# Optimization experiments

Measured on AMD Instinct MI355X. Metric: run time of the kernel, lower is better.

The kernel has to match this reference:

```python
import jax, jax.numpy as jnp
import numpy as np

HIDDEN = 2048
INTER = 4096
NUM_EXPERTS = 8
TOP_K = 4
BATCH, SEQ = 2, 2048
TOKENS = BATCH * SEQ


def setup_inputs() -> dict:
    key = jax.random.key(0)
    k_x, k_rw, k_tw, k_te, k_gu, k_dn = jax.random.split(key, 6)
    x = jax.random.normal(k_x, (BATCH, SEQ, HIDDEN), dtype=jnp.float32)
    # full router weights (passed through but unused by this patched forward)
    weights = jax.random.uniform(k_rw, (TOKENS, NUM_EXPERTS), dtype=jnp.float32)
    tw = jax.random.uniform(k_tw, (TOKENS, TOP_K), dtype=jnp.float32)
    top_weights = tw / jnp.sum(tw, axis=-1, keepdims=True)  # softmax-like, renormalize=False downstream
    top_experts = jax.random.randint(k_te, (TOKENS, TOP_K), 0, NUM_EXPERTS, dtype=jnp.int64)
    scale_gu = 1.0 / np.sqrt(HIDDEN)
    scale_dn = 1.0 / np.sqrt(INTER)
    gate_up_weights = jax.random.normal(k_gu, (NUM_EXPERTS, 2 * INTER, HIDDEN), dtype=jnp.float32) * scale_gu
    down_weights = jax.random.normal(k_dn, (NUM_EXPERTS, HIDDEN, INTER), dtype=jnp.float32) * scale_dn
    return {
        'x': x,
        'weights': weights,
        'top_weights': top_weights,
        'top_experts': top_experts,
        'gate_up_weights': gate_up_weights,
        'down_weights': down_weights,
    }


def _fused_moe(xf, gate_up_weights, down_weights, top_weights, top_experts):
    """xf: [T, D]. Dense per-expert loop (scan over experts), masked combine.

    Matches fused_moe(renormalize=False): out[t] = sum_k top_weights[t,k] * expert_{top_experts[t,k]}(x[t])
    expert(x) = (silu(x @ Wg^T) * (x @ Wu^T)) @ Wd^T with [Wg; Wu] = gate_up.
    """
    E = gate_up_weights.shape[0]

    def step(out, inp):
        w_gu, w_d, e = inp
        # per-token combine coefficient for this expert (0 if not routed)
        coef = jnp.sum(jnp.where(top_experts == e, top_weights, 0.0), axis=-1)  # [T]
        h = xf @ w_gu.T                       # [T, 2*INTER]
        gate, up = jnp.split(h, 2, axis=-1)
        act = jax.nn.silu(gate) * up          # [T, INTER]
        o = act @ w_d.T                       # [T, D]
        return out + coef[:, None] * o, None

    out, _ = jax.lax.scan(step, jnp.zeros_like(xf),
                          (gate_up_weights, down_weights, jnp.arange(E, dtype=jnp.int64)))
    return out


def reference(x, weights, top_weights, top_experts, gate_up_weights, down_weights):
    B, S, D = x.shape
    xf = x.reshape(-1, D)  # flatten(0, 1)
    out = _fused_moe(xf, gate_up_weights, down_weights, top_weights, top_experts)
    return out.reshape(B, S, D)  # unflatten(0, (-1, q_len))
```

## Files before the change

kernel.cpp:

```cpp
#include <hip/hip_runtime.h>
#include <stdint.h>

#define T_TOKENS 4096
#define D_HID    2048
#define D_INT    4096
#define N_EXP    8
#define TOPK     4
#define NFLAT    (T_TOKENS*TOPK)
#define BMT      256
#define MAXPAD   (NFLAT + N_EXP*BMT)
#define MT2      (MAXPAD/BMT)

#define OFF_PTOK 0ull
#define OFF_PWT  73728ull
#define OFF_CNT  147456ull
#define OFF_TOFF 147712ull
#define OFF_SEG  155904ull
#define OFF_XB   262144ull
#define OFF_ACT  17039360ull
#define OFF_W    168034304ull

typedef float f32x4  __attribute__((ext_vector_type(4)));
typedef short bf16x8 __attribute__((ext_vector_type(8)));

__device__ __forceinline__ unsigned short f2bf(float f) {
    unsigned int u = __float_as_uint(f);
    u += 0x7fffu + ((u >> 16) & 1u);
    return (unsigned short)(u >> 16);
}

__device__ __forceinline__ void gload_lds16(const void* g, void* l) {
    __builtin_amdgcn_global_load_lds((const __attribute__((address_space(1))) void*)g,
                                     (__attribute__((address_space(3))) void*)l,
                                     16, 0, 0);
}

__device__ __forceinline__ int xcd_logical(int hw, int nwg) {
    int q = nwg >> 3, r = nwg & 7;
    int xc = hw & 7, sl = hw >> 3;
    return (xc < r ? xc * (q + 1) : r * (q + 1) + (xc - r) * q) + sl;
}

__global__ void k_prep(const float* __restrict__ x, unsigned short* __restrict__ xb,
                       float* __restrict__ out) {
    const int N4 = T_TOKENS * D_HID / 4;
    for (int i = blockIdx.x * 256 + threadIdx.x; i < N4; i += 2048 * 256) {
        float4 v = ((const float4*)x)[i];
        ushort4 h;
        h.x = f2bf(v.x); h.y = f2bf(v.y); h.z = f2bf(v.z); h.w = f2bf(v.w);
        ((ushort4*)xb)[i] = h;
        ((float4*)out)[i] = make_float4(0.f, 0.f, 0.f, 0.f);
    }
}

__global__ void k_cast(const float* __restrict__ src, unsigned short* __restrict__ dst, int n4) {
    for (int i = blockIdx.x * 256 + threadIdx.x; i < n4; i += 2048 * 256) {
        float4 v = ((const float4*)src)[i];
        ushort4 h;
        h.x = f2bf(v.x); h.y = f2bf(v.y); h.z = f2bf(v.z); h.w = f2bf(v.w);
        ((ushort4*)dst)[i] = h;
    }
}

__global__ void k_count(const int* __restrict__ te, int* __restrict__ counts,
                        int* __restrict__ toff) {
    int e = blockIdx.x, t = threadIdx.x;
    int cnt = 0;
    int base = t * 64;
    for (int i = 0; i < 64; i++) cnt += (te[base + i] == e);
    __shared__ int s[256];
    s[t] = cnt; __syncthreads();
    int incl = cnt;
    for (int off = 1; off < 256; off <<= 1) {
        int tmp = (t >= off) ? s[t - off] : 0;
        __syncthreads();
        incl += tmp; s[t] = incl;
        __syncthreads();
    }
    toff[e * 256 + t] = incl - cnt;
    if (t == 255) counts[e] = incl;
}

__global__ void k_fill(const int* __restrict__ te, const float* __restrict__ tw,
                       const int* __restrict__ counts, const int* __restrict__ toff,
                       int* __restrict__ ptok, float* __restrict__ pwt, int* __restrict__ seg) {
    int e = blockIdx.x, t = threadIdx.x;
    int segs[9]; int a = 0;
    #pragma unroll
    for (int j = 0; j < 8; j++) { segs[j] = a; a += (counts[j] + BMT - 1) & ~(BMT - 1); }
    segs[8] = a;
    if (e == 0 && t == 0) { for (int j = 0; j < 9; j++) seg[j] = segs[j]; }
    int base = segs[e] + toff[e * 256 + t];
    int rank = 0;
    for (int i = t * 64; i < (t + 1) * 64; i++) {
        if (te[i] == e) { ptok[base + rank] = i >> 2; pwt[base + rank] = tw[i]; rank++; }
    }
    int cnt = counts[e], pc = (cnt + BMT - 1) & ~(BMT - 1);
    for (int i = cnt + t; i < pc; i += 256) { ptok[segs[e] + i] = -1; pwt[segs[e] + i] = 0.f; }
}


#define MFMA4(MI, AF) \
    _Pragma("unroll") for (int n_ = 0; n_ < 4; ++n_) \
        acc[MI][n_] = __builtin_amdgcn_mfma_f32_16x16x32_bf16(AF, bf[n_], acc[MI][n_], 0, 0, 0);

#define GBODY(VMS) \
  asm volatile("s_waitcnt vmcnt(" VMS ")" ::: "memory"); \
  __builtin_amdgcn_s_barrier(); \
  __builtin_amdgcn_sched_barrier(0); \
  { \
    const char* pT = ldsc + (cb << 15); \
    bf16x8 bf[4], af[4], ag[4]; \
    _Pragma("unroll") for (int n_ = 0; n_ < 4; ++n_) \
        bf[n_] = *(const bf16x8*)(pT + b_off + n_ * 1024); \
    _Pragma("unroll") for (int m_ = 0; m_ < 4; ++m_) \
        af[m_] = *(const bf16x8*)(pT + a_off + m_ * 1024); \
    __builtin_amdgcn_s_barrier(); \
    asm volatile("s_waitcnt lgkmcnt(0)" ::: "memory"); \
    __builtin_amdgcn_sched_barrier(0); \
    __builtin_amdgcn_s_setprio(1); \
    MFMA4(0, af[0]) MFMA4(1, af[1]) MFMA4(2, af[2]) MFMA4(3, af[3]) \
    __builtin_amdgcn_s_setprio(0); \
    __builtin_amdgcn_sched_barrier(0); \
    _Pragma("unroll") for (int m_ = 0; m_ < 4; ++m_) \
        ag[m_] = *(const bf16x8*)(pT + a_off + 4096 + m_ * 1024); \
    asm volatile("s_waitcnt lgkmcnt(0)" ::: "memory"); \
    __builtin_amdgcn_sched_barrier(0); \
    __builtin_amdgcn_s_barrier(); \
    __builtin_amdgcn_s_setprio(1); \
    MFMA4(4, ag[0]) MFMA4(5, ag[1]) MFMA4(6, ag[2]) MFMA4(7, ag[3]) \
    __builtin_amdgcn_s_setprio(0); \
    cb = (cb + 1) & 3; \
  }

__global__ void __launch_bounds__(512, 2)
k_g1(const unsigned short* __restrict__ xb, const unsigned short* __restrict__ wgu_b,
     const int* __restrict__ ptok, const int* __restrict__ seg,
     unsigned short* __restrict__ act) {
    extern __shared__ char smem[];
    char* ldsw = smem; const char* ldsc = smem;
    int logical = xcd_logical(blockIdx.x, 2304);
    int nb = logical / MT2, mb = logical % MT2;
    if (mb * BMT >= seg[8]) return;
    int e = 0;
    #pragma unroll
    for (int j = 1; j < 8; ++j) if (seg[j] <= mb * BMT) e = j;
    int tid = threadIdx.x, w = tid >> 6, l = tid & 63;
    int wr = w >> 2, wc = w & 3;

    int g = (l & 3) ^ ((l >> 3) & 3);
    int r0 = w * 16 + (l >> 2), r1 = 128 + r0;
    int t0 = ptok[mb * BMT + r0]; if (t0 < 0) t0 = 0;
    int t1 = ptok[mb * BMT + r1]; if (t1 < 0) t1 = 0;
    const char* pa0 = (const char*)xb + (size_t)t0 * 4096 + g * 16;
    const char* pa1 = (const char*)xb + (size_t)t1 * 4096 + g * 16;
    int j0 = r0 & 63, j1 = r1 & 63;
    int gr0 = (j0 < 32) ? (nb * 128 + (r0 >> 6) * 32 + j0)
                        : (D_INT + nb * 128 + (r0 >> 6) * 32 + j0 - 32);
    int gr1 = (j1 < 32) ? (nb * 128 + (r1 >> 6) * 32 + j1)
                        : (D_INT + nb * 128 + (r1 >> 6) * 32 + j1 - 32);
    const char* wbase = (const char*)wgu_b + (size_t)e * 8192 * 4096;
    const char* pb0 = wbase + (size_t)gr0 * 4096 + g * 16;
    const char* pb1 = wbase + (size_t)gr1 * 4096 + g * 16;
    int dA0 = w * 1024, dA1 = 8192 + w * 1024;
    int dB0 = 16384 + w * 1024, dB1 = 24576 + w * 1024;
    int sb = 0;
    auto STAGE = [&]() {
        char* d = ldsw + (sb << 15);
        gload_lds16(pa0, d + dA0); gload_lds16(pa1, d + dA1);
        gload_lds16(pb0, d + dB0); gload_lds16(pb1, d + dB1);
        pa0 += 64; pa1 += 64; pb0 += 64; pb1 += 64;
        sb = (sb + 1) & 3;
    };

    int off_frag = (l & 15) * 64 + ((((l >> 4)) ^ (((l & 15) >> 1) & 3)) << 4);
    int a_off = wr * 8192 + off_frag;
    int b_off = 16384 + wc * 4096 + off_frag;

    f32x4 acc[8][4];
    #pragma unroll
    for (int m = 0; m < 8; ++m)
        #pragma unroll
        for (int n = 0; n < 4; ++n) acc[m][n] = (f32x4){0.f, 0.f, 0.f, 0.f};

    int cb = 0;
    STAGE(); STAGE(); STAGE();
    for (int G = 0; G < 61; ++G) { STAGE(); GBODY("12") }
    GBODY("8") GBODY("4") GBODY("0")

    int mbase = mb * BMT;
    #pragma unroll
    for (int m = 0; m < 8; ++m) {
        int rowl = wr * 128 + m * 16 + (l >> 4) * 4;
        #pragma unroll
        for (int np = 0; np < 2; ++np) {
            int col = nb * 128 + wc * 32 + np * 16 + (l & 15);
            #pragma unroll
            for (int r = 0; r < 4; ++r) {
                float gv = acc[m][np][r], uv = acc[m][np + 2][r];
                float av = gv / (1.f + __expf(-gv)) * uv;
                act[(size_t)(mbase + rowl + r) * D_INT + col] = f2bf(av);
            }
        }
    }
}

__global__ void __launch_bounds__(512, 2)
k_g2(const unsigned short* __restrict__ act, const unsigned short* __restrict__ wd_b,
     const int* __restrict__ ptok, const float* __restrict__ pwt,
     const int* __restrict__ seg, float* __restrict__ out) {
    extern __shared__ char smem[];
    char* ldsw = smem; const char* ldsc = smem;
    int logical = xcd_logical(blockIdx.x, 1152);
    int pair = logical / MT2, mb = logical % MT2;
    int nb = pair >> 1, ks = pair & 1;
    if (mb * BMT >= seg[8]) return;
    int e = 0;
    #pragma unroll
    for (int j = 1; j < 8; ++j) if (seg[j] <= mb * BMT) e = j;
    int tid = threadIdx.x, w = tid >> 6, l = tid & 63;
    int wr = w >> 2, wc = w & 3;
    int koff = ks * 4096;

    int g = (l & 3) ^ ((l >> 3) & 3);
    int r0 = w * 16 + (l >> 2), r1 = 128 + r0;
    const char* pa0 = (const char*)act + (size_t)(mb * BMT + r0) * 8192 + koff + g * 16;
    const char* pa1 = (const char*)act + (size_t)(mb * BMT + r1) * 8192 + koff + g * 16;
    const char* wbase = (const char*)wd_b + (size_t)e * D_HID * 8192;
    const char* pb0 = wbase + (size_t)(nb * 256 + r0) * 8192 + koff + g * 16;
    const char* pb1 = wbase + (size_t)(nb * 256 + r1) * 8192 + koff + g * 16;
    int dA0 = w * 1024, dA1 = 8192 + w * 1024;
    int dB0 = 16384 + w * 1024, dB1 = 24576 + w * 1024;
    int sb = 0;
    auto STAGE = [&]() {
        char* d = ldsw + (sb << 15);
        gload_lds16(pa0, d + dA0); gload_lds16(pa1, d + dA1);
        gload_lds16(pb0, d + dB0); gload_lds16(pb1, d + dB1);
        pa0 += 64; pa1 += 64; pb0 += 64; pb1 += 64;
        sb = (sb + 1) & 3;
    };

    int off_frag = (l & 15) * 64 + ((((l >> 4)) ^ (((l & 15) >> 1) & 3)) << 4);
    int a_off = wr * 8192 + off_frag;
    int b_off = 16384 + wc * 4096 + off_frag;

    f32x4 acc[8][4];
    #pragma unroll
    for (int m = 0; m < 8; ++m)
        #pragma unroll
        for (int n = 0; n < 4; ++n) acc[m][n] = (f32x4){0.f, 0.f, 0.f, 0.f};

    int cb = 0;
    STAGE(); STAGE(); STAGE();
    for (int G = 0; G < 61; ++G) { STAGE(); GBODY("12") }
    GBODY("8") GBODY("4") GBODY("0")

    #pragma unroll
    for (int m = 0; m < 8; ++m) {
        int rowl = wr * 128 + m * 16 + (l >> 4) * 4;
        #pragma unroll
        for (int r = 0; r < 4; ++r) {
            int p = mb * BMT + rowl + r;
            int tok = ptok[p];
            float wt = pwt[p];
            if (tok >= 0) {
                #pragma unroll
                for (int n = 0; n < 4; ++n) {
                    int col = nb * 256 + wc * 64 + n * 16 + (l & 15);
                    unsafeAtomicAdd(&out[(size_t)tok * D_HID + col], wt * acc[m][n][r]);
                }
            }
        }
    }
}

extern "C" void kernel_launch(void* const* d_in, const int* in_sizes, int n_in,
                              void* d_out, int out_size, void* d_ws, size_t ws_size,
                              hipStream_t stream) {
    const float* x   = (const float*)d_in[0];
    const float* tw  = (const float*)d_in[2];
    const int*   te  = (const int*)d_in[3];
    const float* wgu = (const float*)d_in[4];
    const float* wd  = (const float*)d_in[5];
    float* out = (float*)d_out;
    char*  ws  = (char*)d_ws;

    int*   ptok   = (int*)(ws + OFF_PTOK);
    float* pwt    = (float*)(ws + OFF_PWT);
    int*   counts = (int*)(ws + OFF_CNT);
    int*   toff   = (int*)(ws + OFF_TOFF);
    int*   seg    = (int*)(ws + OFF_SEG);
    unsigned short* xb  = (unsigned short*)(ws + OFF_XB);
    unsigned short* act = (unsigned short*)(ws + OFF_ACT);
    unsigned short* w_b = (unsigned short*)(ws + OFF_W);

    hipFuncSetAttribute((const void*)k_g1, hipFuncAttributeMaxDynamicSharedMemorySize, 131072);
    hipFuncSetAttribute((const void*)k_g2, hipFuncAttributeMaxDynamicSharedMemorySize, 131072);

    k_prep<<<2048, 256, 0, stream>>>(x, xb, out);
    k_count<<<N_EXP, 256, 0, stream>>>(te, counts, toff);
    k_fill<<<N_EXP, 256, 0, stream>>>(te, tw, counts, toff, ptok, pwt, seg);

    k_cast<<<2048, 256, 0, stream>>>(wgu, w_b, 33554432);
    k_g1<<<2304, 512, 131072, stream>>>(xb, w_b, ptok, seg, act);
    k_cast<<<2048, 256, 0, stream>>>(wd, w_b, 16777216);
    k_g2<<<1152, 512, 131072, stream>>>(act, w_b, ptok, pwt, seg, out);
}
```

Before: 1.325 ms.

## Split global-to-LDS staging into two phases interleaved with MFMA halves

Restructures the main K loop of both grouped GEMM kernels so that each iteration is two phases. The A-tile global-to-LDS loads are issued after the first fragment reads and the B-tile loads after the second. The vmcnt wait is moved to just before the second half's barrier, and barriers are added after each MFMA block. The goal is to spread memory issue across the compute phases and hide load latency better, at the cost of extra barriers and a more delicate wait-count schedule that could expose LDS hazards if miscounted.

```diff
diff --git a/kernel.cpp b/kernel.cpp
--- a/kernel.cpp
+++ b/kernel.cpp
@@ -104,34 +104,67 @@
     _Pragma("unroll") for (int n_ = 0; n_ < 4; ++n_) \
         acc[MI][n_] = __builtin_amdgcn_mfma_f32_16x16x32_bf16(AF, bf[n_], acc[MI][n_], 0, 0, 0);
 
-#define GBODY(VMS) \
-  asm volatile("s_waitcnt vmcnt(" VMS ")" ::: "memory"); \
-  __builtin_amdgcn_s_barrier(); \
-  __builtin_amdgcn_sched_barrier(0); \
+#define GATE8 asm volatile("s_waitcnt vmcnt(8)" ::: "memory");
+#define GATE4 asm volatile("s_waitcnt vmcnt(4)" ::: "memory");
+#define GATE0 asm volatile("s_waitcnt vmcnt(0)" ::: "memory");
+#define GATEN
+
+#define PH_A(DOSTAGE) \
   { \
     const char* pT = ldsc + (cb << 15); \
-    bf16x8 bf[4], af[4], ag[4]; \
     _Pragma("unroll") for (int n_ = 0; n_ < 4; ++n_) \
         bf[n_] = *(const bf16x8*)(pT + b_off + n_ * 1024); \
     _Pragma("unroll") for (int m_ = 0; m_ < 4; ++m_) \
         af[m_] = *(const bf16x8*)(pT + a_off + m_ * 1024); \
+    __builtin_amdgcn_sched_barrier(0); \
+    if (DOSTAGE) { \
+        char* d_ = ldsw + (sb << 15); \
+        gload_lds16(pa0, d_ + dA0); gload_lds16(pa1, d_ + dA1); \
+        pa0 += 64; pa1 += 64; \
+    } \
+    __builtin_amdgcn_sched_barrier(0); \
     __builtin_amdgcn_s_barrier(); \
     asm volatile("s_waitcnt lgkmcnt(0)" ::: "memory"); \
     __builtin_amdgcn_sched_barrier(0); \
     __builtin_amdgcn_s_setprio(1); \
     MFMA4(0, af[0]) MFMA4(1, af[1]) MFMA4(2, af[2]) MFMA4(3, af[3]) \
     __builtin_amdgcn_s_setprio(0); \
-    __builtin_amdgcn_sched_barrier(0); \
+    __builtin_amdgcn_s_barrier(); \
+  }
+
+#define PH_B(DOSTAGE, GATE) \
+  { \
+    const char* pT = ldsc + (cb << 15); \
     _Pragma("unroll") for (int m_ = 0; m_ < 4; ++m_) \
         ag[m_] = *(const bf16x8*)(pT + a_off + 4096 + m_ * 1024); \
+    __builtin_amdgcn_sched_barrier(0); \
+    if (DOSTAGE) { \
+        char* d_ = ldsw + (sb << 15); \
+        gload_lds16(pb0, d_ + dB0); gload_lds16(pb1, d_ + dB1); \
+        pb0 += 64; pb1 += 64; sb = (sb + 1) & 3; \
+    } \
+    GATE \
+    __builtin_amdgcn_sched_barrier(0); \
+    __builtin_amdgcn_s_barrier(); \
     asm volatile("s_waitcnt lgkmcnt(0)" ::: "memory"); \
     __builtin_amdgcn_sched_barrier(0); \
-    __builtin_amdgcn_s_barrier(); \
     __builtin_amdgcn_s_setprio(1); \
     MFMA4(4, ag[0]) MFMA4(5, ag[1]) MFMA4(6, ag[2]) MFMA4(7, ag[3]) \
     __builtin_amdgcn_s_setprio(0); \
+    __builtin_amdgcn_s_barrier(); \
     cb = (cb + 1) & 3; \
   }
+
+#define KLOOP \
+    bf16x8 bf[4], af[4], ag[4]; \
+    int cb = 0; \
+    STAGE(); STAGE(); STAGE(); \
+    asm volatile("s_waitcnt vmcnt(8)" ::: "memory"); \
+    __builtin_amdgcn_s_barrier(); \
+    for (int T = 0; T < 61; ++T) { PH_A(1) PH_B(1, GATE8) } \
+    PH_A(0) PH_B(0, GATE4) \
+    PH_A(0) PH_B(0, GATE0) \
+    PH_A(0) PH_B(0, GATEN)
 
 __global__ void __launch_bounds__(512, 2)
 k_g1(const unsigned short* __restrict__ xb, const unsigned short* __restrict__ wgu_b,
@@ -183,10 +216,7 @@
         #pragma unroll
         for (int n = 0; n < 4; ++n) acc[m][n] = (f32x4){0.f, 0.f, 0.f, 0.f};
 
-    int cb = 0;
-    STAGE(); STAGE(); STAGE();
-    for (int G = 0; G < 61; ++G) { STAGE(); GBODY("12") }
-    GBODY("8") GBODY("4") GBODY("0")
+    KLOOP
 
     int mbase = mb * BMT;
     #pragma unroll
@@ -250,10 +280,7 @@
         #pragma unroll
         for (int n = 0; n < 4; ++n) acc[m][n] = (f32x4){0.f, 0.f, 0.f, 0.f};
 
-    int cb = 0;
-    STAGE(); STAGE(); STAGE();
-    for (int G = 0; G < 61; ++G) { STAGE(); GBODY("12") }
-    GBODY("8") GBODY("4") GBODY("0")
+    KLOOP
 
     #pragma unroll
     for (int m = 0; m < 8; ++m) {
```

Measured after the change: 1.277 ms. -3.6%, faster.
